# Optimization experiments

Hardware: AMD Instinct MI355X
Metric: run time of the kernel (lower is better)

The kernel has to match this reference:

```python
import jax, jax.numpy as jnp
import numpy as np

D_IN, D_OUT, K = 128, 128, 64
X_MIN, X_MAX = 0.0, 1.0
EPS = 1e-12


def _pchip_slopes(y, x):
    # y: [..., K], x: [K] strictly increasing -> slopes [..., K]. Assumes K >= 3.
    h = x[1:] - x[:-1]                      # [K-1]
    delta = (y[..., 1:] - y[..., :-1]) / (h + EPS)
    h0, h1 = h[:-1], h[1:]
    w1 = 2.0 * h1 + h0
    w2 = h1 + 2.0 * h0
    d0_, d1_ = delta[..., :-1], delta[..., 1:]
    same_sign = d0_ * d1_ > 0
    denom = w1 / (d0_ + EPS) + w2 / (d1_ + EPS)
    d_int = jnp.where(same_sign, (w1 + w2) / (denom + EPS), 0.0)  # [..., K-2]
    d_first = ((2.0 * h[0] + h[1]) * delta[..., 0] - h[0] * delta[..., 1]) / (h[0] + h[1] + EPS)
    d_last = ((2.0 * h[-1] + h[-2]) * delta[..., -1] - h[-1] * delta[..., -2]) / (h[-1] + h[-2] + EPS)

    def limit(di, de):
        di = jnp.where(di * de <= 0, 0.0, di)
        return jnp.where(jnp.abs(di) > 3.0 * jnp.abs(de), 3.0 * de, di)

    d_first = limit(d_first, delta[..., 0])
    d_last = limit(d_last, delta[..., -1])
    return jnp.concatenate([d_first[..., None], d_int, d_last[..., None]], axis=-1)


def setup_inputs() -> dict:
    key = jax.random.key(0)
    k1, k2 = jax.random.split(key)
    x = jax.random.normal(k1, (4096, D_IN), dtype=jnp.float32)
    coeffs = 0.2 * jax.random.normal(k2, (D_OUT, D_IN, K), dtype=jnp.float32)
    bias = jnp.zeros((D_OUT,), dtype=jnp.float32)
    knots = jnp.linspace(X_MIN, X_MAX, K, dtype=jnp.float32)
    return {"x": x, "coeffs": coeffs, "bias": bias, "knots": knots}


def reference(x, coeffs, bias, knots):
    B = x.shape[0]
    slopes = _pchip_slopes(coeffs, knots)              # [d_out, d_in, K]
    h = (X_MAX - X_MIN) / (K - 1)

    xc = jnp.clip(x, X_MIN, X_MAX)                     # [B, d_in]
    idx = jnp.clip(jnp.floor((xc - X_MIN) / h).astype(jnp.int32), 0, K - 2)
    t = (xc - (X_MIN + idx.astype(x.dtype) * h)) / h   # [B, d_in]
    t2 = t * t
    t3 = t2 * t
    h00 = 2 * t3 - 3 * t2 + 1
    h10 = t3 - 2 * t2 + t
    h01 = -2 * t3 + 3 * t2
    h11 = t3 - t2

    ct = jnp.transpose(coeffs, (1, 2, 0))              # [d_in, K, d_out]
    dt = jnp.transpose(slopes, (1, 2, 0))              # [d_in, K, d_out]
    ii = jnp.arange(D_IN)[None, :]                     # [1, d_in]
    y0 = ct[ii, idx]                                   # [B, d_in, d_out]
    y1 = ct[ii, idx + 1]
    d0 = dt[ii, idx]
    d1 = dt[ii, idx + 1]

    yi = (h00[..., None] * y0 + h10[..., None] * h * d0
          + h01[..., None] * y1 + h11[..., None] * h * d1)  # [B, d_in, d_out]

    # linear extrapolation beyond the knot range
    y_left = ct[:, 0, :][None] + dt[:, 0, :][None] * (x - X_MIN)[..., None]
    y_right = ct[:, -1, :][None] + dt[:, -1, :][None] * (x - X_MAX)[..., None]
    yi = jnp.where((x < X_MIN)[..., None], y_left, yi)
    yi = jnp.where((x > X_MAX)[..., None], y_right, yi)

    return yi.sum(axis=1) + bias[None, :]              # [B, d_out]
```

## Files before the change

### kernel.cpp

```cpp
#include <hip/hip_runtime.h>

#define KN 64
#define DIN 128
#define DOUT 128
#define EPSF 1e-12f
#define HF (1.0f / 63.0f)

#define SIDE_ELE (128 * 63 * 32)
#define SIDE_DW  (128 * 63 * 128)

typedef _Float16 h2 __attribute__((ext_vector_type(2)));
typedef float    f2 __attribute__((ext_vector_type(2)));

#if defined(__has_builtin)
#if __has_builtin(__builtin_amdgcn_fdot2)
#define FDOT2(a, b, c) __builtin_amdgcn_fdot2((a), (b), (c), false)
#endif
#if __has_builtin(__builtin_amdgcn_cvt_pk_fp8_f32) && __has_builtin(__builtin_amdgcn_cvt_pk_f32_fp8)
#define HAVE_HW_FP8 1
#endif
#endif
#ifndef FDOT2
static __device__ __forceinline__ float FDOT2(h2 a, h2 b, float c) {
    return c + (float)a.x * (float)b.x + (float)a.y * (float)b.y;
}
#endif

#ifndef HAVE_HW_FP8
static __device__ __forceinline__ unsigned enc8(float x) {
    unsigned s = (x < 0.0f) ? 1u : 0u;
    x = fabsf(x);
    x = fminf(x, 448.0f);
    if (x < 0.015625f) {
        unsigned m = (unsigned)(x * 512.0f + 0.5f);
        return (s << 7) | m;
    }
    int e; float fr = frexpf(x, &e);
    int E = e - 1 + 7;
    unsigned m = (unsigned)((2.0f * fr - 1.0f) * 8.0f + 0.5f);
    if (m == 8) { m = 0; ++E; }
    if (E > 15) { E = 15; m = 6; }
    return (s << 7) | ((unsigned)E << 3) | m;
}
static __device__ __forceinline__ float dec8(unsigned b) {
    unsigned s = b >> 7, e = (b >> 3) & 15, m = b & 7;
    float v = (e == 0) ? ldexpf((float)m, -9) : ldexpf(8.0f + (float)m, (int)e - 10);
    return s ? -v : v;
}
#endif

static __device__ __forceinline__ unsigned pack4_fp8(float a, float b, float c, float d) {
#ifdef HAVE_HW_FP8
    int r = __builtin_amdgcn_cvt_pk_fp8_f32(a, b, 0, false);
    r = __builtin_amdgcn_cvt_pk_fp8_f32(c, d, r, true);
    return (unsigned)r;
#else
    return enc8(a) | (enc8(b) << 8) | (enc8(c) << 16) | (enc8(d) << 24);
#endif
}
static __device__ __forceinline__ f2 dec2lo(unsigned u) {
#ifdef HAVE_HW_FP8
    return __builtin_amdgcn_cvt_pk_f32_fp8((int)u, false);
#else
    f2 r; r.x = dec8(u & 255u); r.y = dec8((u >> 8) & 255u); return r;
#endif
}
static __device__ __forceinline__ f2 dec2hi(unsigned u) {
#ifdef HAVE_HW_FP8
    return __builtin_amdgcn_cvt_pk_f32_fp8((int)u, true);
#else
    f2 r; r.x = dec8((u >> 16) & 255u); r.y = dec8((u >> 24) & 255u); return r;
#endif
}


__global__ __launch_bounds__(256) void kan_precompute(
    const float* __restrict__ coeffs,
    const float* __restrict__ knots,
    unsigned int* __restrict__ tb)
{
    const int i      = blockIdx.x >> 1;
    const int o_base = (blockIdx.x & 1) << 6;
    const int wave   = threadIdx.x >> 6;
    const int lane   = threadIdx.x & 63;

    __shared__ float ys[64][65];
    __shared__ float ds[64][65];

    float kn  = knots[lane];
    float kn1 = (lane < 63) ? knots[lane + 1] : 0.0f;
    float hk  = kn1 - kn;
    float hm1 = __shfl_up(hk, 1);
    float h1v = __shfl_down(hk, 1);
    float hm2 = __shfl_up(hk, 2);

    for (int ol = wave; ol < 64; ol += 4) {
        const int o = o_base + ol;
        float y = coeffs[(o * DIN + i) * KN + lane];
        float ynext = __shfl_down(y, 1);
        float delta = (lane < 63) ? (ynext - y) / (hk + EPSF) : 0.0f;
        float dm1 = __shfl_up(delta, 1);

        float w1v = 2.0f * hk + hm1;
        float w2v = hk + 2.0f * hm1;
        float denom = w1v / (dm1 + EPSF) + w2v / (delta + EPSF);
        float d = (dm1 * delta > 0.0f) ? (w1v + w2v) / (denom + EPSF) : 0.0f;

        float d1v = __shfl_down(delta, 1);
        if (lane == 0) {
            float df = ((2.0f * hk + h1v) * delta - hk * d1v) / (hk + h1v + EPSF);
            if (df * delta <= 0.0f) df = 0.0f;
            else if (fabsf(df) > 3.0f * fabsf(delta)) df = 3.0f * delta;
            d = df;
        }
        float dm2 = __shfl_up(delta, 2);
        if (lane == 63) {
            float dl = ((2.0f * hm1 + hm2) * dm1 - hm1 * dm2) / (hm1 + hm2 + EPSF);
            if (dl * dm1 <= 0.0f) dl = 0.0f;
            else if (fabsf(dl) > 3.0f * fabsf(dm1)) dl = 3.0f * dm1;
            d = dl;
        }
        ys[ol][lane] = y;
        ds[ol][lane] = d * HF;
    }
    __syncthreads();

    const int ol = threadIdx.x & 63;
    const int o  = o_base + ol;
    for (int j = threadIdx.x >> 6; j < 63; j += 4) {
        tb[(i * 63 + j) * 128 + o] =
            pack4_fp8(ys[ol][j], ds[ol][j], ys[ol][j + 1], ds[ol][j + 1]);
    }
    if (threadIdx.x < 128) {
        const int side = threadIdx.x >> 6;
        const int k    = side ? 63 : 0;
        h2 v; v.x = (_Float16)ys[ol][k]; v.y = (_Float16)ds[ol][k];
        tb[SIDE_DW + (i * 2 + side) * 128 + o] = __builtin_bit_cast(unsigned int, v);
    }
}

__global__ __launch_bounds__(256) void kan_main(
    const float* __restrict__ x,
    const uint4* __restrict__ tb4,
    const float* __restrict__ bias,
    float* __restrict__ out)
{
    const int b0   = blockIdx.x << 1;
    const int tid  = threadIdx.x;
    const int wv   = tid >> 6;
    const int bl   = wv >> 1;
    const int w2   = wv & 1;
    const int lane = tid & 63;
    const int hw   = lane >> 5;
    const int q32  = lane & 31;

    __shared__ float4 wlw[2][DIN];
    __shared__ uint2  wlo[2][DIN];
    __shared__ float4 red[2][32];

    {
        const int bl1 = tid >> 7;
        const int i1  = tid & 127;
        float xv = x[(b0 + bl1) * DIN + i1];
        float4 w; unsigned base, cls; unsigned w01p = 0;
        if (xv < 0.0f || xv > 1.0f) {
            const int side = (xv > 1.0f) ? 1 : 0;
            float tt = (xv - (side ? 1.0f : 0.0f)) * 63.0f;
            w = make_float4(1.0f, tt, 0.0f, 0.0f);
            base = (unsigned)(SIDE_ELE + ((i1 * 2 + side) << 5));
            cls = 1u;
            h2 wp; wp.x = (_Float16)1.0f; wp.y = (_Float16)tt;
            w01p = __builtin_bit_cast(unsigned int, wp);
        } else {
            int idx = (int)(xv * 63.0f);
            idx = idx > 62 ? 62 : idx;
            float t = xv * 63.0f - (float)idx;
            float t2 = t * t, t3 = t2 * t;
            w.x = 2.0f * t3 - 3.0f * t2 + 1.0f;
            w.y = t3 - 2.0f * t2 + t;
            w.z = 3.0f * t2 - 2.0f * t3;
            w.w = t3 - t2;
            base = (unsigned)((i1 * 63 + idx) << 5);
            cls = 0u;
        }
        wlw[bl1][i1] = w;
        uint2 m; m.x = base | (cls << 31); m.y = w01p;
        wlo[bl1][i1] = m;
    }
    __syncthreads();

    float4 acc = make_float4(0.0f, 0.0f, 0.0f, 0.0f);
    const int myib = (w2 << 6) + (hw << 5);

    #pragma unroll 8
    for (int n = 0; n < 32; ++n) {
        float4 w = wlw[bl][myib + n];
        uint2  m = wlo[bl][myib + n];
        uint4  r = tb4[(m.x & 0x7FFFFFFFu) + (unsigned)q32];
        if (m.x >> 31) {
            h2 w01 = __builtin_bit_cast(h2, m.y);
            acc.x = FDOT2(w01, __builtin_bit_cast(h2, r.x), acc.x);
            acc.y = FDOT2(w01, __builtin_bit_cast(h2, r.y), acc.y);
            acc.z = FDOT2(w01, __builtin_bit_cast(h2, r.z), acc.z);
            acc.w = FDOT2(w01, __builtin_bit_cast(h2, r.w), acc.w);
        } else {
            f2 lo, hi;
            lo = dec2lo(r.x); hi = dec2hi(r.x);
            acc.x += w.x * lo.x + w.y * lo.y + w.z * hi.x + w.w * hi.y;
            lo = dec2lo(r.y); hi = dec2hi(r.y);
            acc.y += w.x * lo.x + w.y * lo.y + w.z * hi.x + w.w * hi.y;
            lo = dec2lo(r.z); hi = dec2hi(r.z);
            acc.z += w.x * lo.x + w.y * lo.y + w.z * hi.x + w.w * hi.y;
            lo = dec2lo(r.w); hi = dec2hi(r.w);
            acc.w += w.x * lo.x + w.y * lo.y + w.z * hi.x + w.w * hi.y;
        }
    }

    acc.x += __shfl_xor(acc.x, 32);
    acc.y += __shfl_xor(acc.y, 32);
    acc.z += __shfl_xor(acc.z, 32);
    acc.w += __shfl_xor(acc.w, 32);

    if (w2 == 1 && lane < 32) red[bl][q32] = acc;
    __syncthreads();
    if (w2 == 0 && lane < 32) {
        float4 r2 = red[bl][q32];
        float4 bo = reinterpret_cast<const float4*>(bias)[q32];
        float4 res;
        res.x = acc.x + r2.x + bo.x;
        res.y = acc.y + r2.y + bo.y;
        res.z = acc.z + r2.z + bo.z;
        res.w = acc.w + r2.w + bo.w;
        reinterpret_cast<float4*>(out + (b0 + bl) * DOUT)[q32] = res;
    }
}

extern "C" void kernel_launch(void* const* d_in, const int* in_sizes, int n_in,
                              void* d_out, int out_size, void* d_ws, size_t ws_size,
                              hipStream_t stream) {
    const float* x      = (const float*)d_in[0];
    const float* coeffs = (const float*)d_in[1];
    const float* bias   = (const float*)d_in[2];
    const float* knots  = (const float*)d_in[3];
    float* out = (float*)d_out;
    unsigned int* tb = (unsigned int*)d_ws;

    kan_precompute<<<256, 256, 0, stream>>>(coeffs, knots, tb);
    kan_main<<<2048, 256, 0, stream>>>(x, (const uint4*)tb, bias, out);
}
```

Before: 94.99 us.

## Split output columns across blocks and stage side-table rows in LDS

The packed FP8 table is regrouped into four 32-column output quarters. Each block now handles 16 batch rows for one quarter, with every lane doing all 128 inputs for two outputs. The cross-wave shared-memory reduction is gone. Extrapolation coefficients for the quarter are preloaded into LDS, and the Hermite weights are stored as fp16 pairs. The aim is better reuse of per-block setup and narrower loads, but the LDS footprint grows (about 32KB side table plus weights), both branch results are computed for every input, and the fp16 weights lose some precision.

```diff
diff --git a/kernel.cpp b/kernel.cpp
--- a/kernel.cpp
+++ b/kernel.cpp
@@ -6,8 +6,8 @@
 #define EPSF 1e-12f
 #define HF (1.0f / 63.0f)
 
-#define SIDE_ELE (128 * 63 * 32)
-#define SIDE_DW  (128 * 63 * 128)
+#define SIDE_DW (128 * 63 * 4 * 32)
+#define SIDE_U2 (128 * 63 * 4 * 16)
 
 typedef _Float16 h2 __attribute__((ext_vector_type(2)));
 typedef float    f2 __attribute__((ext_vector_type(2)));
@@ -72,7 +72,6 @@
     f2 r; r.x = dec8((u >> 16) & 255u); r.y = dec8((u >> 24) & 255u); return r;
 #endif
 }
-
 
 __global__ __launch_bounds__(256) void kan_precompute(
     const float* __restrict__ coeffs,
@@ -125,114 +124,112 @@
     }
     __syncthreads();
 
-    const int ol = threadIdx.x & 63;
-    const int o  = o_base + ol;
-    for (int j = threadIdx.x >> 6; j < 63; j += 4) {
-        tb[(i * 63 + j) * 128 + o] =
-            pack4_fp8(ys[ol][j], ds[ol][j], ys[ol][j + 1], ds[ol][j + 1]);
+    {
+        const int ol   = threadIdx.x & 63;
+        const int oq   = (o_base >> 5) + (ol >> 5);
+        const int opos = ol & 31;
+        for (int j = threadIdx.x >> 6; j < 63; j += 4) {
+            tb[(((i * 63 + j) << 2) + oq) * 32 + opos] =
+                pack4_fp8(ys[ol][j], ds[ol][j], ys[ol][j + 1], ds[ol][j + 1]);
+        }
     }
     if (threadIdx.x < 128) {
         const int side = threadIdx.x >> 6;
+        const int ol   = threadIdx.x & 63;
+        const int oq   = (o_base >> 5) + (ol >> 5);
+        const int opos = ol & 31;
         const int k    = side ? 63 : 0;
         h2 v; v.x = (_Float16)ys[ol][k]; v.y = (_Float16)ds[ol][k];
-        tb[SIDE_DW + (i * 2 + side) * 128 + o] = __builtin_bit_cast(unsigned int, v);
+        tb[SIDE_DW + (((oq << 7) + i) * 2 + side) * 32 + opos] =
+            __builtin_bit_cast(unsigned int, v);
     }
 }
 
 __global__ __launch_bounds__(256) void kan_main(
     const float* __restrict__ x,
-    const uint4* __restrict__ tb4,
+    const uint2* __restrict__ tbu2,
     const float* __restrict__ bias,
     float* __restrict__ out)
 {
-    const int b0   = blockIdx.x << 1;
-    const int tid  = threadIdx.x;
-    const int wv   = tid >> 6;
-    const int bl   = wv >> 1;
-    const int w2   = wv & 1;
-    const int lane = tid & 63;
-    const int hw   = lane >> 5;
-    const int q32  = lane & 31;
-
-    __shared__ float4 wlw[2][DIN];
-    __shared__ uint2  wlo[2][DIN];
-    __shared__ float4 red[2][32];
+    const int bg  = blockIdx.x >> 2;
+    const int oq  = blockIdx.x & 3;
+    const int b0  = bg << 4;
+    const int tid = threadIdx.x;
+    const int w   = tid >> 6;
+    const int ln  = tid & 63;
+    const int p   = ln >> 4;
+    const int l16 = ln & 15;
+    const int bl  = (w << 2) + p;
+
+    __shared__ uint2 sW[16][130];
+    __shared__ uint  sO[16][130];
+    __shared__ uint2 sSide[4096];
 
     {
-        const int bl1 = tid >> 7;
-        const int i1  = tid & 127;
+        const uint2* gs = tbu2 + SIDE_U2 + (oq << 12);
+        #pragma unroll
+        for (int k = 0; k < 16; ++k)
+            sSide[tid + (k << 8)] = gs[tid + (k << 8)];
+    }
+
+    #pragma unroll
+    for (int q = tid; q < 16 * DIN; q += 256) {
+        const int bl1 = q >> 7;
+        const int i1  = q & 127;
         float xv = x[(b0 + bl1) * DIN + i1];
-        float4 w; unsigned base, cls; unsigned w01p = 0;
+        uint2 wp; unsigned ow;
         if (xv < 0.0f || xv > 1.0f) {
             const int side = (xv > 1.0f) ? 1 : 0;
             float tt = (xv - (side ? 1.0f : 0.0f)) * 63.0f;
-            w = make_float4(1.0f, tt, 0.0f, 0.0f);
-            base = (unsigned)(SIDE_ELE + ((i1 * 2 + side) << 5));
-            cls = 1u;
-            h2 wp; wp.x = (_Float16)1.0f; wp.y = (_Float16)tt;
-            w01p = __builtin_bit_cast(unsigned int, wp);
+            h2 w01; w01.x = (_Float16)1.0f; w01.y = (_Float16)tt;
+            wp.x = __builtin_bit_cast(unsigned int, w01);
+            wp.y = 0u;
+            ow = (unsigned)(((i1 << 1) + side) << 4) | 0x80000000u;
         } else {
             int idx = (int)(xv * 63.0f);
             idx = idx > 62 ? 62 : idx;
             float t = xv * 63.0f - (float)idx;
             float t2 = t * t, t3 = t2 * t;
-            w.x = 2.0f * t3 - 3.0f * t2 + 1.0f;
-            w.y = t3 - 2.0f * t2 + t;
-            w.z = 3.0f * t2 - 2.0f * t3;
-            w.w = t3 - t2;
-            base = (unsigned)((i1 * 63 + idx) << 5);
-            cls = 0u;
-        }
-        wlw[bl1][i1] = w;
-        uint2 m; m.x = base | (cls << 31); m.y = w01p;
-        wlo[bl1][i1] = m;
+            h2 w01; w01.x = (_Float16)(2.0f * t3 - 3.0f * t2 + 1.0f);
+            w01.y = (_Float16)(t3 - 2.0f * t2 + t);
+            h2 w23; w23.x = (_Float16)(3.0f * t2 - 2.0f * t3);
+            w23.y = (_Float16)(t3 - t2);
+            wp.x = __builtin_bit_cast(unsigned int, w01);
+            wp.y = __builtin_bit_cast(unsigned int, w23);
+            ow = (unsigned)((((i1 * 63 + idx) << 2) + oq) << 4);
+        }
+        sW[bl1][i1] = wp;
+        sO[bl1][i1] = ow;
     }
     __syncthreads();
 
-    float4 acc = make_float4(0.0f, 0.0f, 0.0f, 0.0f);
-    const int myib = (w2 << 6) + (hw << 5);
-
+    float acc0 = 0.0f, acc1 = 0.0f;
     #pragma unroll 8
-    for (int n = 0; n < 32; ++n) {
-        float4 w = wlw[bl][myib + n];
-        uint2  m = wlo[bl][myib + n];
-        uint4  r = tb4[(m.x & 0x7FFFFFFFu) + (unsigned)q32];
-        if (m.x >> 31) {
-            h2 w01 = __builtin_bit_cast(h2, m.y);
-            acc.x = FDOT2(w01, __builtin_bit_cast(h2, r.x), acc.x);
-            acc.y = FDOT2(w01, __builtin_bit_cast(h2, r.y), acc.y);
-            acc.z = FDOT2(w01, __builtin_bit_cast(h2, r.z), acc.z);
-            acc.w = FDOT2(w01, __builtin_bit_cast(h2, r.w), acc.w);
-        } else {
-            f2 lo, hi;
-            lo = dec2lo(r.x); hi = dec2hi(r.x);
-            acc.x += w.x * lo.x + w.y * lo.y + w.z * hi.x + w.w * hi.y;
-            lo = dec2lo(r.y); hi = dec2hi(r.y);
-            acc.y += w.x * lo.x + w.y * lo.y + w.z * hi.x + w.w * hi.y;
-            lo = dec2lo(r.z); hi = dec2hi(r.z);
-            acc.z += w.x * lo.x + w.y * lo.y + w.z * hi.x + w.w * hi.y;
-            lo = dec2lo(r.w); hi = dec2hi(r.w);
-            acc.w += w.x * lo.x + w.y * lo.y + w.z * hi.x + w.w * hi.y;
-        }
-    }
-
-    acc.x += __shfl_xor(acc.x, 32);
-    acc.y += __shfl_xor(acc.y, 32);
-    acc.z += __shfl_xor(acc.z, 32);
-    acc.w += __shfl_xor(acc.w, 32);
-
-    if (w2 == 1 && lane < 32) red[bl][q32] = acc;
-    __syncthreads();
-    if (w2 == 0 && lane < 32) {
-        float4 r2 = red[bl][q32];
-        float4 bo = reinterpret_cast<const float4*>(bias)[q32];
-        float4 res;
-        res.x = acc.x + r2.x + bo.x;
-        res.y = acc.y + r2.y + bo.y;
-        res.z = acc.z + r2.z + bo.z;
-        res.w = acc.w + r2.w + bo.w;
-        reinterpret_cast<float4*>(out + (b0 + bl) * DOUT)[q32] = res;
-    }
+    for (int i = 0; i < DIN; ++i) {
+        uint2 wp = sW[bl][i];
+        unsigned ow = sO[bl][i];
+        const bool isExt = (ow >> 31) != 0u;
+        const unsigned off = ow & 0x7FFFFFFFu;
+        uint2 g  = tbu2[(isExt ? 0u : off) + (unsigned)l16];
+        uint2 sd = sSide[(isExt ? off : 0u) + (unsigned)l16];
+        h2 w01 = __builtin_bit_cast(h2, wp.x);
+        h2 w23 = __builtin_bit_cast(h2, wp.y);
+        float w0 = (float)w01.x, w1 = (float)w01.y;
+        float w2 = (float)w23.x, w3 = (float)w23.y;
+        f2 lo0 = dec2lo(g.x), hi0 = dec2hi(g.x);
+        f2 lo1 = dec2lo(g.y), hi1 = dec2hi(g.y);
+        float rI0 = w0 * lo0.x + w1 * lo0.y + w2 * hi0.x + w3 * hi0.y;
+        float rI1 = w0 * lo1.x + w1 * lo1.y + w2 * hi1.x + w3 * hi1.y;
+        float rE0 = FDOT2(w01, __builtin_bit_cast(h2, sd.x), 0.0f);
+        float rE1 = FDOT2(w01, __builtin_bit_cast(h2, sd.y), 0.0f);
+        acc0 += isExt ? rE0 : rI0;
+        acc1 += isExt ? rE1 : rI1;
+    }
+
+    const int o2 = (oq << 4) + l16;
+    float2 bo = reinterpret_cast<const float2*>(bias)[o2];
+    float2 res; res.x = acc0 + bo.x; res.y = acc1 + bo.y;
+    reinterpret_cast<float2*>(out + (b0 + bl) * DOUT)[o2] = res;
 }
 
 extern "C" void kernel_launch(void* const* d_in, const int* in_sizes, int n_in,
@@ -246,5 +243,5 @@
     unsigned int* tb = (unsigned int*)d_ws;
 
     kan_precompute<<<256, 256, 0, stream>>>(coeffs, knots, tb);
-    kan_main<<<2048, 256, 0, stream>>>(x, (const uint4*)tb, bias, out);
-}
+    kan_main<<<1024, 256, 0, stream>>>(x, (const uint2*)tb, bias, out);
+}
```

Result: slower. 116.5 us (+22.6%).
